# Optimization experiments

Hardware: AMD Instinct MI355X
Metric: run time of the kernel (lower is better)

The kernel has to match this reference:

```python
import jax, jax.numpy as jnp
import numpy as np

GROUPS = 32
EPS = 1e-5


def _group_norm(x, scale, bias):
    B, C, H, W = x.shape
    xg = x.reshape(B, GROUPS, -1)
    mu = xg.mean(axis=-1, keepdims=True)
    var = jnp.mean(jnp.square(xg - mu), axis=-1, keepdims=True)
    xn = ((xg - mu) * jax.lax.rsqrt(var + EPS)).reshape(B, C, H, W)
    return xn * scale[None, :, None, None] + bias[None, :, None, None]


def _conv1x1(x, w, b):
    # x: [B,C,H,W], w: [O,C], b: [O]
    return jnp.einsum('bchw,oc->bohw', x, w) + b[None, :, None, None]


def setup_inputs() -> dict:
    key = jax.random.key(0)
    ks = jax.random.split(key, 6)
    B, C, H, W = 16, 512, 32, 32
    x = jax.random.normal(ks[0], (B, C, H, W), dtype=jnp.float32)
    # xavier_uniform for [C, C, 1, 1] conv: limit = sqrt(6 / (fan_in + fan_out)) = sqrt(6 / (2C))
    lim = float(np.sqrt(6.0 / (2 * C)))
    wq = jax.random.uniform(ks[1], (C, C), jnp.float32, -lim, lim)
    wk = jax.random.uniform(ks[2], (C, C), jnp.float32, -lim, lim)
    wv = jax.random.uniform(ks[3], (C, C), jnp.float32, -lim, lim)
    wo = jax.random.uniform(ks[4], (C, C), jnp.float32, -lim, lim) * 1e-5  # gain=1e-5
    zeros_c = jnp.zeros((C,), jnp.float32)
    return {
        'x': x,
        'gn_scale': jnp.ones((C,), jnp.float32),
        'gn_bias': zeros_c,
        'wq': wq, 'bq': zeros_c,
        'wk': wk, 'bk': zeros_c,
        'wv': wv, 'bv': zeros_c,
        'wo': wo, 'bo': zeros_c,
    }


def reference(x, gn_scale, gn_bias, wq, bq, wk, bk, wv, bv, wo, bo):
    B, C, H, W = x.shape
    N = H * W
    h = _group_norm(x, gn_scale, gn_bias)
    q = _conv1x1(h, wq, bq).reshape(B, C, N)  # [B,C,N]
    k = _conv1x1(h, wk, bk).reshape(B, C, N)
    v = _conv1x1(h, wv, bv).reshape(B, C, N)
    scale = 1.0 / jnp.sqrt(jnp.asarray(C, x.dtype))
    w = jnp.einsum('bcn,bcm->bnm', q, k) * scale  # [B,N,N]
    w = jax.nn.softmax(w, axis=-1)
    hv = jnp.einsum('bnm,bcm->bcn', w, v).reshape(B, C, H, W)
    out = _conv1x1(hv, wo, bo)
    return x + out
```

## Files before the change

kernel.cpp:

```cpp
#include <hip/hip_runtime.h>
#include <hip/hip_bf16.h>
#include <cstdint>

typedef unsigned char u8;
typedef float floatx4 __attribute__((ext_vector_type(4)));
typedef int intx8 __attribute__((ext_vector_type(8)));

__device__ __forceinline__ void gld_lds16(const void* g, void* l) {
    __builtin_amdgcn_global_load_lds(
        (const __attribute__((address_space(1))) unsigned int*)g,
        (__attribute__((address_space(3))) unsigned int*)l, 16, 0, 0);
}

__device__ __forceinline__ u8 f2fp8(float v) {
    return (u8)(__builtin_amdgcn_cvt_pk_fp8_f32(v, v, 0, false) & 0xff);
}
__device__ __forceinline__ unsigned int pack4_fp8(float a, float b, float c, float d) {
    unsigned int u = __builtin_amdgcn_cvt_pk_fp8_f32(a, b, 0, false);
    u = __builtin_amdgcn_cvt_pk_fp8_f32(c, d, u, true);
    return u;
}

__device__ __forceinline__ intx8 ld_frag(const u8* p, int lo, int hi) {
    uint4 a = *(const uint4*)(p + lo);
    uint4 b = *(const uint4*)(p + hi);
    intx8 r;
    r[0] = a.x; r[1] = a.y; r[2] = a.z; r[3] = a.w;
    r[4] = b.x; r[5] = b.y; r[6] = b.z; r[7] = b.w;
    return r;
}

__global__ __launch_bounds__(256) void setup_kernel(
    const float* __restrict__ x, const float* __restrict__ gs,
    const float* __restrict__ gb,
    const float* __restrict__ wq, const float* __restrict__ wk,
    const float* __restrict__ wv, const float* __restrict__ wo,
    const float* __restrict__ bq, const float* __restrict__ bk,
    const float* __restrict__ bv,
    u8* __restrict__ hT, u8* __restrict__ wqkv, u8* __restrict__ wob,
    float* __restrict__ bqkv, float* __restrict__ lsum)
{
    const int t = threadIdx.x;
    if (blockIdx.x >= 512) {
        int i = (blockIdx.x - 512) * 256 + t;
        if (i < 786432) {
            int which = i >> 18;
            int off = i & 262143;
            const float* src = which == 0 ? wq : which == 1 ? wk : wv;
            wqkv[i] = f2fp8(src[off]);
        } else {
            wob[i - 786432] = f2fp8(wo[i - 786432] * 262144.0f);
        }
        if (i < 1536)
            bqkv[i] = i < 512 ? bq[i] : (i < 1024 ? bk[i - 512] : bv[i - 1024]);
        if (i < 16384)
            lsum[i] = 0.0f;
        return;
    }
    const int b = blockIdx.x >> 5;
    const int g = blockIdx.x & 31;
    const int wave = t >> 6, lane = t & 63;
    const float4* x4 = (const float4*)(x + ((long long)b * 512 + g * 16) * 1024);

    float4 v[16];
    float s1 = 0.f, s2 = 0.f;
#pragma unroll
    for (int i = 0; i < 16; ++i) {
        v[i] = x4[i * 256 + t];
        s1 += v[i].x + v[i].y + v[i].z + v[i].w;
        s2 += v[i].x * v[i].x + v[i].y * v[i].y + v[i].z * v[i].z + v[i].w * v[i].w;
    }
#pragma unroll
    for (int m = 32; m; m >>= 1) {
        s1 += __shfl_xor(s1, m, 64);
        s2 += __shfl_xor(s2, m, 64);
    }
    __shared__ float red[2][4];
    __shared__ float stats[2];
    if (lane == 0) { red[0][wave] = s1; red[1][wave] = s2; }
    __syncthreads();
    if (t == 0) {
        float a = red[0][0] + red[0][1] + red[0][2] + red[0][3];
        float q = red[1][0] + red[1][1] + red[1][2] + red[1][3];
        float mu = a * (1.0f / 16384.0f);
        float var = q * (1.0f / 16384.0f) - mu * mu;
        stats[0] = mu;
        stats[1] = rsqrtf(var + 1e-5f);
    }
    __syncthreads();
    const float mu = stats[0], rs = stats[1];

#pragma unroll
    for (int i = 0; i < 16; ++i) {
        const float sc = gs[g * 16 + i] * rs;
        const float bi = gb[g * 16 + i] - mu * sc;
        v[i].x = v[i].x * sc + bi;
        v[i].y = v[i].y * sc + bi;
        v[i].z = v[i].z * sc + bi;
        v[i].w = v[i].w * sc + bi;
    }
    u8* hb = hT + (long long)b * 524288 + g * 16;
#pragma unroll
    for (int r = 0; r < 4; ++r) {
        uint4 o;
        o.x = pack4_fp8(v[0][r],  v[1][r],  v[2][r],  v[3][r]);
        o.y = pack4_fp8(v[4][r],  v[5][r],  v[6][r],  v[7][r]);
        o.z = pack4_fp8(v[8][r],  v[9][r],  v[10][r], v[11][r]);
        o.w = pack4_fp8(v[12][r], v[13][r], v[14][r], v[15][r]);
        *(uint4*)(hb + (long long)(4 * t + r) * 512) = o;
    }
}

template <int EPI>
__global__ __launch_bounds__(256, 3) void gemm_mx(
    const u8* __restrict__ A, long long sA,
    const u8* __restrict__ B, long long sB,
    void* __restrict__ C, long long sC,
    void* __restrict__ C2, void* __restrict__ C3,
    int ldC, int K,
    const float* __restrict__ bias,
    const float* __restrict__ resid, long long sR,
    float scale, float* __restrict__ lsum)
{
    __shared__ __align__(16) u8 smem[33792];
    const int tid = threadIdx.x;
    const int l = tid & 63;
    const int wave = tid >> 6;
    const int wm = wave >> 1, wn = wave & 1;
    const int bm = blockIdx.x, bn = blockIdx.y, b = blockIdx.z;

    const u8* Ab = A + (long long)b * sA + (long long)bm * 128 * K;
    const u8* Bb = B + (long long)b * sB + (long long)bn * 128 * K;

    const int srow = wave * 8 + (l >> 3);
    const int sg = ((l & 7) ^ ((l >> 3) & 7)) * 16;
    const u8* ga  = Ab + (long long)srow * K + sg;
    const u8* gbp = Bb + (long long)srow * K + sg;
    const long long c32 = (long long)32 * K;
    const int ldst = wave * 1024;

    const int q4 = l >> 4;
    const int glo = ((2 * q4) ^ (l & 7)) * 16;
    const int ghi = ((2 * q4 + 1) ^ (l & 7)) * 16;
    int arow[4], brow[4];
#pragma unroll
    for (int i = 0; i < 4; ++i) {
        arow[i] = (wm * 64 + i * 16 + (l & 15)) * 128;
        brow[i] = (wn * 64 + i * 16 + (l & 15)) * 128 + 16384;
    }

    floatx4 acc[4][4] = {};
    const int niter = K >> 7;

    for (int it = 0; it < niter; ++it) {
        const int k0 = it << 7;
#pragma unroll
        for (int c = 0; c < 4; ++c) {
            gld_lds16(ga + c * c32 + k0, smem + c * 4096 + ldst);
            gld_lds16(gbp + c * c32 + k0, smem + 16384 + c * 4096 + ldst);
        }
        __syncthreads();
        intx8 bfr[4];
#pragma unroll
        for (int j = 0; j < 4; ++j) bfr[j] = ld_frag(smem + brow[j], glo, ghi);
#pragma unroll
        for (int i = 0; i < 4; ++i) {
            intx8 af = ld_frag(smem + arow[i], glo, ghi);
#pragma unroll
            for (int j = 0; j < 4; ++j)
                acc[i][j] = __builtin_amdgcn_mfma_scale_f32_16x16x128_f8f6f4(
                    af, bfr[j], acc[i][j], 0, 0, 0, 127, 0, 127);
        }
        __syncthreads();
    }

    if (EPI == 3) {
        float* Cf = (float*)C;
#pragma unroll
        for (int i = 0; i < 4; ++i) {
            const int mrow = bm * 128 + wm * 64 + i * 16 + q4 * 4;
#pragma unroll
            for (int j = 0; j < 4; ++j) {
                const int ncol = bn * 128 + wn * 64 + j * 16 + (l & 15);
#pragma unroll
                for (int r = 0; r < 4; ++r) {
                    const int row = mrow + r;
                    float v = acc[i][j][r] * scale + bias[row] +
                              resid[(long long)b * sR + (long long)row * ldC + ncol];
                    Cf[(long long)b * sC + (long long)row * ldC + ncol] = v;
                }
            }
        }
    } else if (EPI == 1) {
        const int which = bn >> 2;
        u8* tile = smem;
#pragma unroll
        for (int i = 0; i < 4; ++i) {
            const int rl = wm * 64 + i * 16 + q4 * 4;
#pragma unroll
            for (int j = 0; j < 4; ++j) {
                const int cl = wn * 64 + j * 16 + (l & 15);
                const float badd = bias[bn * 128 + cl];
                if (which == 2) {
                    *(unsigned int*)(tile + cl * 144 + rl) =
                        pack4_fp8(acc[i][j][0] + badd, acc[i][j][1] + badd,
                                  acc[i][j][2] + badd, acc[i][j][3] + badd);
                } else {
#pragma unroll
                    for (int r = 0; r < 4; ++r)
                        tile[(rl + r) * 144 + cl] = f2fp8(acc[i][j][r] + badd);
                }
            }
        }
        __syncthreads();
        const int slot = (tid & 7) * 16;
#pragma unroll
        for (int p = 0; p < 4; ++p) {
            const int row = p * 32 + (tid >> 3);
            uint4 d = *(const uint4*)(tile + row * 144 + slot);
            u8* dst;
            if (which == 0)
                dst = (u8*)C + (long long)b * sC + (long long)(bm * 128 + row) * 512
                      + (bn & 3) * 128 + slot;
            else if (which == 1)
                dst = (u8*)C2 + (long long)b * sC + (long long)(bm * 128 + row) * 512
                      + (bn & 3) * 128 + slot;
            else
                dst = (u8*)C3 + (long long)b * sC + (long long)((bn & 3) * 128 + row) * 1024
                      + bm * 128 + slot;
            *(uint4*)dst = d;
        }
    } else if (EPI == 4) {
        u8* tile = smem;
#pragma unroll
        for (int i = 0; i < 4; ++i) {
            const int rl = wm * 64 + i * 16 + q4 * 4;
            float psum[4] = {0.f, 0.f, 0.f, 0.f};
#pragma unroll
            for (int j = 0; j < 4; ++j) {
                const int cl = wn * 64 + j * 16 + (l & 15);
#pragma unroll
                for (int r = 0; r < 4; ++r) {
                    float e = __expf(acc[i][j][r] * scale);
                    psum[r] += e;
                    tile[(rl + r) * 144 + cl] = f2fp8(e * 0.25f);
                }
            }
#pragma unroll
            for (int r = 0; r < 4; ++r) {
#pragma unroll
                for (int m = 8; m; m >>= 1) psum[r] += __shfl_xor(psum[r], m, 64);
            }
            if ((l & 15) == 0) {
                float* lp = lsum + b * 1024 + bm * 128 + rl;
#pragma unroll
                for (int r = 0; r < 4; ++r) atomicAdd(lp + r, psum[r]);
            }
        }
        __syncthreads();
        const int slot = (tid & 7) * 16;
#pragma unroll
        for (int p = 0; p < 4; ++p) {
            const int row = p * 32 + (tid >> 3);
            uint4 d = *(const uint4*)(tile + row * 144 + slot);
            u8* dst = (u8*)C + (long long)b * sC + (long long)(bm * 128 + row) * ldC
                      + bn * 128 + slot;
            *(uint4*)dst = d;
        }
    } else {
        u8* tile = smem;
#pragma unroll
        for (int i = 0; i < 4; ++i) {
            const int rl = wm * 64 + i * 16 + q4 * 4;
            const float* lp = lsum + b * 1024 + bm * 128 + rl;
            float rc[4];
#pragma unroll
            for (int r = 0; r < 4; ++r) rc[r] = 4.0f / lp[r];
#pragma unroll
            for (int j = 0; j < 4; ++j) {
                const int cl = wn * 64 + j * 16 + (l & 15);
#pragma unroll
                for (int r = 0; r < 4; ++r)
                    tile[(rl + r) * 144 + cl] = f2fp8(acc[i][j][r] * rc[r]);
            }
        }
        __syncthreads();
        const int slot = (tid & 7) * 16;
#pragma unroll
        for (int p = 0; p < 4; ++p) {
            const int row = p * 32 + (tid >> 3);
            uint4 d = *(const uint4*)(tile + row * 144 + slot);
            u8* dst = (u8*)C + (long long)b * sC + (long long)(bm * 128 + row) * ldC
                      + bn * 128 + slot;
            *(uint4*)dst = d;
        }
    }
}

extern "C" void kernel_launch(void* const* d_in, const int* in_sizes, int n_in,
                              void* d_out, int out_size, void* d_ws, size_t ws_size,
                              hipStream_t stream)
{
    const float* x  = (const float*)d_in[0];
    const float* gs = (const float*)d_in[1];
    const float* gb = (const float*)d_in[2];
    const float* wq = (const float*)d_in[3];
    const float* bq = (const float*)d_in[4];
    const float* wk = (const float*)d_in[5];
    const float* bk = (const float*)d_in[6];
    const float* wv = (const float*)d_in[7];
    const float* bv = (const float*)d_in[8];
    const float* wo = (const float*)d_in[9];
    const float* bo = (const float*)d_in[10];
    float* out = (float*)d_out;

    u8* p = (u8*)d_ws;
    u8* hT   = p; p += 8388608;
    u8* q    = p; p += 8388608;
    u8* k    = p; p += 8388608;
    u8* v    = p; p += 8388608;
    u8* wqkv = p; p += 786432;
    float* bqkv = (float*)p; p += 6144;
    u8* wob  = p; p += 262144;
    u8* P    = p; p += 16777216;
    u8* hvT  = p; p += 8388608;
    float* lsum = (float*)p; p += 65536;

    setup_kernel<<<4608, 256, 0, stream>>>(x, gs, gb, wq, wk, wv, wo, bq, bk, bv,
                                           hT, wqkv, wob, bqkv, lsum);

    gemm_mx<1><<<dim3(8, 12, 16), 256, 0, stream>>>(
        hT, 524288LL, wqkv, 0LL, q, 524288LL, k, v,
        512, 512, bqkv, nullptr, 0LL, 1.0f, nullptr);
    gemm_mx<4><<<dim3(8, 8, 16), 256, 0, stream>>>(
        q, 524288LL, k, 524288LL, P, 1048576LL, nullptr, nullptr,
        1024, 512, nullptr, nullptr, 0LL, 0.044194173824159216f, lsum);
    gemm_mx<5><<<dim3(8, 4, 16), 256, 0, stream>>>(
        P, 1048576LL, v, 524288LL, hvT, 524288LL, nullptr, nullptr,
        512, 1024, nullptr, nullptr, 0LL, 1.0f, lsum);
    gemm_mx<3><<<dim3(4, 8, 16), 256, 0, stream>>>(
        wob, 0LL, hvT, 524288LL, out, 524288LL, nullptr, nullptr,
        1024, 512, bo, x, 524288LL, 3.814697265625e-06f, nullptr);
}
```

Baseline: 176.7 us.

## Fuse QK^T, softmax and PV into a single attention kernel

Replaces the two attention GEMM launches with one fused kernel, `attn_fused`. Each block keeps a 64-row Q tile in LDS, streams K and V tiles through a staging buffer, and exponentiates scores in registers. It repacks the probabilities to fp8 in LDS and accumulates the output in registers, then normalizes by a per-row sum reduced within the block. This removes the 16 MB fp8 P matrix round trip, the global atomics on lsum, and the lsum zeroing. The cost is only 256 blocks with a large register accumulator and LDS footprint, and K/V loads that are synchronised rather than double-buffered, so latency hiding may be weak.

```diff
diff --git a/kernel.cpp b/kernel.cpp
--- a/kernel.cpp
+++ b/kernel.cpp
@@ -38,7 +38,7 @@
     const float* __restrict__ bq, const float* __restrict__ bk,
     const float* __restrict__ bv,
     u8* __restrict__ hT, u8* __restrict__ wqkv, u8* __restrict__ wob,
-    float* __restrict__ bqkv, float* __restrict__ lsum)
+    float* __restrict__ bqkv)
 {
     const int t = threadIdx.x;
     if (blockIdx.x >= 512) {
@@ -53,8 +53,6 @@
         }
         if (i < 1536)
             bqkv[i] = i < 512 ? bq[i] : (i < 1024 ? bk[i - 512] : bv[i - 1024]);
-        if (i < 16384)
-            lsum[i] = 0.0f;
         return;
     }
     const int b = blockIdx.x >> 5;
@@ -120,7 +118,7 @@
     int ldC, int K,
     const float* __restrict__ bias,
     const float* __restrict__ resid, long long sR,
-    float scale, float* __restrict__ lsum)
+    float scale)
 {
     __shared__ __align__(16) u8 smem[33792];
     const int tid = threadIdx.x;
@@ -191,7 +189,7 @@
                 }
             }
         }
-    } else if (EPI == 1) {
+    } else {
         const int which = bn >> 2;
         u8* tile = smem;
 #pragma unroll
@@ -230,70 +228,137 @@
                       + bm * 128 + slot;
             *(uint4*)dst = d;
         }
-    } else if (EPI == 4) {
-        u8* tile = smem;
-#pragma unroll
-        for (int i = 0; i < 4; ++i) {
-            const int rl = wm * 64 + i * 16 + q4 * 4;
-            float psum[4] = {0.f, 0.f, 0.f, 0.f};
-#pragma unroll
-            for (int j = 0; j < 4; ++j) {
-                const int cl = wn * 64 + j * 16 + (l & 15);
-#pragma unroll
-                for (int r = 0; r < 4; ++r) {
-                    float e = __expf(acc[i][j][r] * scale);
-                    psum[r] += e;
-                    tile[(rl + r) * 144 + cl] = f2fp8(e * 0.25f);
+    }
+}
+
+__global__ __launch_bounds__(256, 2) void attn_fused(
+    const u8* __restrict__ q, const u8* __restrict__ k,
+    const u8* __restrict__ v, u8* __restrict__ hvT)
+{
+    __shared__ __align__(16) u8 smem[73728];
+    const int tid = threadIdx.x;
+    const int l = tid & 63;
+    const int wave = tid >> 6;
+    const int qq = l >> 4;
+    const int bm = blockIdx.x, b = blockIdx.y;
+    const u8* qb = q + (long long)b * 524288;
+    const u8* kb = k + (long long)b * 524288;
+    const u8* vb = v + (long long)b * 524288;
+    const float SC = 0.044194173824159216f;
+
+    {
+        const int rbase = wave * 2 + (l >> 5);
+        const int cc = (l >> 3) & 3;
+        const int s = l & 7;
+#pragma unroll
+        for (int c = 0; c < 8; ++c) {
+            const int row = c * 8 + rbase;
+            const int g = s ^ (row & 7);
+            gld_lds16(qb + (long long)(bm * 64 + row) * 512 + cc * 128 + g * 16,
+                      smem + c * 4096 + wave * 1024);
+        }
+    }
+
+    const int glo = ((2 * qq) ^ (l & 7)) * 16;
+    const int ghi = ((2 * qq + 1) ^ (l & 7)) * 16;
+    const int srow = wave * 8 + (l >> 3);
+    const int fg = ((l & 7) ^ ((l >> 3) & 7)) * 16;
+    u8* stg = smem + 32768;
+    u8* slds = smem + 65536 + wave * 2048;
+    const int qrow = (wave * 16 + (l & 15)) * 512;
+
+    floatx4 oacc[32] = {};
+    float lpart = 0.f;
+
+    for (int mt = 0; mt < 8; ++mt) {
+        const int m0 = mt * 128;
+        floatx4 sacc[8] = {};
+#pragma unroll 1
+        for (int rnd = 0; rnd < 2; ++rnd) {
+#pragma unroll
+            for (int h = 0; h < 2; ++h) {
+                const int cc = rnd * 2 + h;
+#pragma unroll
+                for (int c = 0; c < 4; ++c)
+                    gld_lds16(kb + (long long)(m0 + c * 32 + srow) * 512 + cc * 128 + fg,
+                              stg + h * 16384 + c * 4096 + wave * 1024);
+            }
+            __syncthreads();
+#pragma unroll
+            for (int h = 0; h < 2; ++h) {
+                const int cc = rnd * 2 + h;
+                intx8 qf = ld_frag(smem + qrow + cc * 128, glo, ghi);
+                const u8* base = stg + h * 16384;
+#pragma unroll
+                for (int i = 0; i < 8; ++i) {
+                    intx8 af = ld_frag(base + (i * 16 + (l & 15)) * 128, glo, ghi);
+                    sacc[i] = __builtin_amdgcn_mfma_scale_f32_16x16x128_f8f6f4(
+                        af, qf, sacc[i], 0, 0, 0, 127, 0, 127);
                 }
             }
-#pragma unroll
-            for (int r = 0; r < 4; ++r) {
-#pragma unroll
-                for (int m = 8; m; m >>= 1) psum[r] += __shfl_xor(psum[r], m, 64);
-            }
-            if ((l & 15) == 0) {
-                float* lp = lsum + b * 1024 + bm * 128 + rl;
-#pragma unroll
-                for (int r = 0; r < 4; ++r) atomicAdd(lp + r, psum[r]);
-            }
-        }
-        __syncthreads();
-        const int slot = (tid & 7) * 16;
-#pragma unroll
-        for (int p = 0; p < 4; ++p) {
-            const int row = p * 32 + (tid >> 3);
-            uint4 d = *(const uint4*)(tile + row * 144 + slot);
-            u8* dst = (u8*)C + (long long)b * sC + (long long)(bm * 128 + row) * ldC
-                      + bn * 128 + slot;
-            *(uint4*)dst = d;
-        }
-    } else {
-        u8* tile = smem;
-#pragma unroll
-        for (int i = 0; i < 4; ++i) {
-            const int rl = wm * 64 + i * 16 + q4 * 4;
-            const float* lp = lsum + b * 1024 + bm * 128 + rl;
-            float rc[4];
-#pragma unroll
-            for (int r = 0; r < 4; ++r) rc[r] = 4.0f / lp[r];
-#pragma unroll
-            for (int j = 0; j < 4; ++j) {
-                const int cl = wn * 64 + j * 16 + (l & 15);
-#pragma unroll
-                for (int r = 0; r < 4; ++r)
-                    tile[(rl + r) * 144 + cl] = f2fp8(acc[i][j][r] * rc[r]);
-            }
-        }
-        __syncthreads();
-        const int slot = (tid & 7) * 16;
-#pragma unroll
-        for (int p = 0; p < 4; ++p) {
-            const int row = p * 32 + (tid >> 3);
-            uint4 d = *(const uint4*)(tile + row * 144 + slot);
-            u8* dst = (u8*)C + (long long)b * sC + (long long)(bm * 128 + row) * ldC
-                      + bn * 128 + slot;
-            *(uint4*)dst = d;
-        }
+            __syncthreads();
+        }
+#pragma unroll
+        for (int i = 0; i < 8; ++i) {
+            float e0 = __expf(sacc[i][0] * SC);
+            float e1 = __expf(sacc[i][1] * SC);
+            float e2 = __expf(sacc[i][2] * SC);
+            float e3 = __expf(sacc[i][3] * SC);
+            lpart += (e0 + e1) + (e2 + e3);
+            *(unsigned int*)(slds + (l & 15) * 128 + ((i ^ (l & 7)) * 16) + qq * 4) =
+                pack4_fp8(e0 * 0.25f, e1 * 0.25f, e2 * 0.25f, e3 * 0.25f);
+        }
+        intx8 pf = ld_frag(slds + (l & 15) * 128, glo, ghi);
+#pragma unroll 1
+        for (int rnd = 0; rnd < 2; ++rnd) {
+#pragma unroll
+            for (int h = 0; h < 2; ++h) {
+                const int c0 = (rnd * 2 + h) * 128;
+#pragma unroll
+                for (int c = 0; c < 4; ++c)
+                    gld_lds16(vb + (long long)(c0 + c * 32 + srow) * 1024 + m0 + fg,
+                              stg + h * 16384 + c * 4096 + wave * 1024);
+            }
+            __syncthreads();
+#pragma unroll
+            for (int h = 0; h < 2; ++h) {
+                const int cch = rnd * 2 + h;
+                const u8* base = stg + h * 16384;
+#pragma unroll
+                for (int j = 0; j < 8; ++j) {
+                    intx8 bf = ld_frag(base + (j * 16 + (l & 15)) * 128, glo, ghi);
+                    oacc[cch * 8 + j] = __builtin_amdgcn_mfma_scale_f32_16x16x128_f8f6f4(
+                        pf, bf, oacc[cch * 8 + j], 0, 0, 0, 127, 0, 127);
+                }
+            }
+            __syncthreads();
+        }
+    }
+
+    lpart += __shfl_xor(lpart, 16, 64);
+    lpart += __shfl_xor(lpart, 32, 64);
+    float rn[4];
+#pragma unroll
+    for (int r = 0; r < 4; ++r)
+        rn[r] = 4.0f / __shfl(lpart, qq * 4 + r, 64);
+
+#pragma unroll
+    for (int t32 = 0; t32 < 32; ++t32) {
+        const int cbyte = (t32 >> 3) * 128 + (t32 & 7) * 16 + (l & 15);
+        const int nb = (wave * 16 + qq * 4) * 512 + cbyte;
+#pragma unroll
+        for (int r = 0; r < 4; ++r)
+            smem[nb + r * 512] = f2fp8(oacc[t32][r] * rn[r]);
+    }
+    __syncthreads();
+    const int rrow = tid >> 5;
+    const int cb16 = (tid & 31) * 16;
+    u8* hb = hvT + (long long)b * 524288 + (long long)bm * 64 * 512;
+#pragma unroll
+    for (int c = 0; c < 8; ++c) {
+        const int rr = c * 8 + rrow;
+        uint4 d = *(const uint4*)(smem + rr * 512 + cb16);
+        *(uint4*)(hb + rr * 512 + cb16) = d;
     }
 }
 
@@ -322,23 +387,15 @@
     u8* wqkv = p; p += 786432;
     float* bqkv = (float*)p; p += 6144;
     u8* wob  = p; p += 262144;
-    u8* P    = p; p += 16777216;
     u8* hvT  = p; p += 8388608;
-    float* lsum = (float*)p; p += 65536;
 
     setup_kernel<<<4608, 256, 0, stream>>>(x, gs, gb, wq, wk, wv, wo, bq, bk, bv,
-                                           hT, wqkv, wob, bqkv, lsum);
-
+                                           hT, wqkv, wob, bqkv);
     gemm_mx<1><<<dim3(8, 12, 16), 256, 0, stream>>>(
         hT, 524288LL, wqkv, 0LL, q, 524288LL, k, v,
-        512, 512, bqkv, nullptr, 0LL, 1.0f, nullptr);
-    gemm_mx<4><<<dim3(8, 8, 16), 256, 0, stream>>>(
-        q, 524288LL, k, 524288LL, P, 1048576LL, nullptr, nullptr,
-        1024, 512, nullptr, nullptr, 0LL, 0.044194173824159216f, lsum);
-    gemm_mx<5><<<dim3(8, 4, 16), 256, 0, stream>>>(
-        P, 1048576LL, v, 524288LL, hvT, 524288LL, nullptr, nullptr,
-        512, 1024, nullptr, nullptr, 0LL, 1.0f, lsum);
+        512, 512, bqkv, nullptr, 0LL, 1.0f);
+    attn_fused<<<dim3(16, 16), 256, 0, stream>>>(q, k, v, hvT);
     gemm_mx<3><<<dim3(4, 8, 16), 256, 0, stream>>>(
         wob, 0LL, hvT, 524288LL, out, 524288LL, nullptr, nullptr,
-        1024, 512, bo, x, 524288LL, 3.814697265625e-06f, nullptr);
-}
+        1024, 512, bo, x, 524288LL, 3.814697265625e-06f);
+}
```

New measurement: 251.8 us. 1.42x slower.
